# Optimization experiments

Hardware: AMD Instinct MI355X
Metric: run time of the kernel (lower is better)

The kernel has to match this reference:

```python
import jax, jax.numpy as jnp
import numpy as np

EMBED, HEADS, DEPTH = 1280, 16, 2
HD = EMBED // HEADS            # 80
MLP = 4 * EMBED                # 5120
HIDDEN = 3584
MERGE = 2
PATCH_IN = 3 * 2 * 14 * 14     # 1176
GRIDS = [(1, 32, 32), (1, 32, 32)]
SEQ = sum(t * h * w for t, h, w in GRIDS)  # 2048
THETA = 10000.0


def _pos_ids_np():
    m = MERGE
    out = []
    for t, h, w in GRIDS:
        hp = np.broadcast_to(np.arange(h)[:, None], (h, w))
        hp = hp.reshape(h // m, m, w // m, m).transpose(0, 2, 1, 3).reshape(-1)
        wp = np.broadcast_to(np.arange(w)[None, :], (h, w))
        wp = wp.reshape(h // m, m, w // m, m).transpose(0, 2, 1, 3).reshape(-1)
        out.append(np.tile(np.stack([hp, wp], -1), (t, 1)))
    return np.concatenate(out, 0).astype(np.int32)


def _cu_seqlens_np():
    lens = []
    for t, h, w in GRIDS:
        lens += [h * w] * t
    return np.concatenate([[0], np.cumsum(lens)]).astype(np.int32)


def setup_inputs() -> dict:
    key = jax.random.key(0)
    ks = iter(jax.random.split(key, 16))
    s = 0.02
    p = {}
    p["hidden_states"] = jax.random.normal(next(ks), (SEQ, PATCH_IN), jnp.float32)
    p["pos_ids"] = jnp.asarray(_pos_ids_np())
    p["cu_seqlens"] = jnp.asarray(_cu_seqlens_np())
    p["patch_w"] = jax.random.normal(next(ks), (PATCH_IN, EMBED)) * s
    p["ln1_w"] = jnp.ones((DEPTH, EMBED)); p["ln1_b"] = jnp.zeros((DEPTH, EMBED))
    p["ln2_w"] = jnp.ones((DEPTH, EMBED)); p["ln2_b"] = jnp.zeros((DEPTH, EMBED))
    p["qkv_w"] = jax.random.normal(next(ks), (DEPTH, EMBED, 3 * EMBED)) * s
    p["qkv_b"] = jnp.zeros((DEPTH, 3 * EMBED))
    p["proj_w"] = jax.random.normal(next(ks), (DEPTH, EMBED, EMBED)) * s
    p["proj_b"] = jnp.zeros((DEPTH, EMBED))
    p["fc1_w"] = jax.random.normal(next(ks), (DEPTH, EMBED, MLP)) * s
    p["fc1_b"] = jnp.zeros((DEPTH, MLP))
    p["fc2_w"] = jax.random.normal(next(ks), (DEPTH, MLP, EMBED)) * s
    p["fc2_b"] = jnp.zeros((DEPTH, EMBED))
    p["mrg_ln_w"] = jnp.ones((EMBED,)); p["mrg_ln_b"] = jnp.zeros((EMBED,))
    p["mrg_w1"] = jax.random.normal(next(ks), (EMBED * MERGE * MERGE, HIDDEN)) * s
    p["mrg_b1"] = jnp.zeros((HIDDEN,))
    p["mrg_w2"] = jax.random.normal(next(ks), (HIDDEN, HIDDEN)) * s
    p["mrg_b2"] = jnp.zeros((HIDDEN,))
    return p


def _ln(x, w, b, eps=1e-6):
    mu = jnp.mean(x, -1, keepdims=True)
    var = jnp.mean((x - mu) ** 2, -1, keepdims=True)
    return (x - mu) * jax.lax.rsqrt(var + eps) * w + b


def _rotate_half(x):
    x1, x2 = jnp.split(x, 2, axis=-1)
    return jnp.concatenate([-x2, x1], axis=-1)


def reference(hidden_states, pos_ids, cu_seqlens, patch_w, ln1_w, ln1_b, ln2_w,
              ln2_b, qkv_w, qkv_b, proj_w, proj_b, fc1_w, fc1_b, fc2_w, fc2_b,
              mrg_ln_w, mrg_ln_b, mrg_w1, mrg_b1, mrg_w2, mrg_b2):
    # patch embed (Conv3d with full-patch kernel == linear on flattened patch)
    x = hidden_states @ patch_w                              # [S, E]

    # vision rotary embedding over (h, w) position ids
    inv_freq = 1.0 / THETA ** (jnp.arange(0, HD // 2, 2, dtype=jnp.float32) / (HD // 2))  # [HD//4]
    freqs = pos_ids.astype(jnp.float32)[:, :, None] * inv_freq  # [S, 2, HD//4]
    freqs = freqs.reshape(SEQ, -1)                           # [S, HD//2]
    emb = jnp.concatenate([freqs, freqs], -1)                # [S, HD]
    cos = jnp.cos(emb)[:, None, :]
    sin = jnp.sin(emb)[:, None, :]

    # block-diagonal (per-image) mask from cu_seqlens
    seg = jnp.searchsorted(cu_seqlens[1:], jnp.arange(SEQ), side='right')
    mask = seg[:, None] == seg[None, :]                      # [S, S]

    scale = 1.0 / np.sqrt(HD)
    neg = jnp.finfo(jnp.float32).min
    for i in range(DEPTH):
        h = _ln(x, ln1_w[i], ln1_b[i])
        qkv = (h @ qkv_w[i] + qkv_b[i]).reshape(SEQ, 3, HEADS, HD)
        q, k, v = qkv[:, 0], qkv[:, 1], qkv[:, 2]
        q = q * cos + _rotate_half(q) * sin
        k = k * cos + _rotate_half(k) * sin
        scores = jnp.einsum('qhd,khd->hqk', q, k) * scale    # [H, S, S]
        scores = jnp.where(mask[None], scores, neg)
        attn = jax.nn.softmax(scores.astype(jnp.float32), -1).astype(q.dtype)
        o = jnp.einsum('hqk,khd->qhd', attn, v).reshape(SEQ, EMBED)
        x = x + o @ proj_w[i] + proj_b[i]
        h = _ln(x, ln2_w[i], ln2_b[i])
        x = x + jax.nn.silu(h @ fc1_w[i] + fc1_b[i]) @ fc2_w[i] + fc2_b[i]

    # patch merger: LN then merge 2x2 windows then 2-layer MLP
    y = _ln(x, mrg_ln_w, mrg_ln_b).reshape(-1, EMBED * MERGE * MERGE)
    y = jax.nn.gelu(y @ mrg_w1 + mrg_b1, approximate=False) @ mrg_w2 + mrg_b2
    return y                                                  # [S/4, HIDDEN]
```

## Files before the change

### kernel.cpp

```cpp
#include <hip/hip_runtime.h>
#include <math.h>

#define SEQ    2048
#define EMBED  1280
#define HEADS  16
#define HD     80
#define MLP    5120
#define HIDDEN 3584
#define QKVN   3840
#define SEGLEN 1024
#define NSEG   2
#define PATCH_IN 1176
#define PATCH_KP 1216
#define MROWS  512

typedef __attribute__((ext_vector_type(8))) short bf16x8;
typedef __attribute__((ext_vector_type(4))) float f32x4;
typedef unsigned short ushort_t;

__device__ __forceinline__ ushort_t f2bf(float f) {
    unsigned u = __builtin_bit_cast(unsigned, f);
    unsigned r = u + 0x7FFFu + ((u >> 16) & 1u);
    return (ushort_t)(r >> 16);
}

__device__ __forceinline__ void gld_lds16(const void* g, void* l) {
    __builtin_amdgcn_global_load_lds(
        (const __attribute__((address_space(1))) void*)g,
        (__attribute__((address_space(3))) void*)l, 16, 0, 0);
}

template<int EPI, int ACC, int OBF>
__global__ __launch_bounds__(256) void gemm_bf16(
    const ushort_t* __restrict__ A, const ushort_t* __restrict__ Bt,
    const float* __restrict__ bias, void* __restrict__ Cout,
    int M, int N, int K)
{
    __shared__ __align__(16) short Abuf[2][128 * 64];
    __shared__ __align__(16) short Bbuf[2][128 * 64];

    const int tid  = threadIdx.x;
    const int lane = tid & 63, wid = tid >> 6;
    const int wr = wid >> 1, wc = wid & 1;

    const int nwg  = gridDim.x * gridDim.y;
    const int flat = blockIdx.y * gridDim.x + blockIdx.x;
    int bx, by;
    if (nwg & 7) { bx = blockIdx.x; by = blockIdx.y; }
    else {
        const int swz = (flat & 7) * (nwg >> 3) + (flat >> 3);
        bx = swz % gridDim.x; by = swz / gridDim.x;
    }
    const int row0 = by * 128, col0 = bx * 128;

    const int r0 = tid >> 3, s0 = tid & 7;
    const int lrow = lane & 15;
    const int lg = lane >> 4;
    const int rx = lrow & 7;

    f32x4 acc[4][4] = {};

    auto stage = [&](int buf, int t) {
        const int k0 = t << 6;
        #pragma unroll
        for (int i = 0; i < 4; ++i) {
            const int r = r0 + i * 32;
            const int ksl = (s0 ^ (r & 7)) * 8;
            gld_lds16(A  + (size_t)(row0 + r) * K + k0 + ksl,
                      &Abuf[buf][(tid + i * 256) * 8]);
            gld_lds16(Bt + (size_t)(col0 + r) * K + k0 + ksl,
                      &Bbuf[buf][(tid + i * 256) * 8]);
        }
    };

    const int nt = K >> 6;
    stage(0, 0);
    stage(1, 1);

    int cur = 0;
    for (int t = 0; t < nt; ++t) {
        if (t < nt - 1) { asm volatile("s_waitcnt vmcnt(8)" ::: "memory"); }
        else            { asm volatile("s_waitcnt vmcnt(0)" ::: "memory"); }
        __builtin_amdgcn_s_barrier();

        bf16x8 a[2][4], b[2][4];
        #pragma unroll
        for (int ko = 0; ko < 2; ++ko) {
            const int ts = ((ko * 4 + lg) ^ rx) * 8;
            #pragma unroll
            for (int m = 0; m < 4; ++m)
                a[ko][m] = *(const bf16x8*)&Abuf[cur][(wr * 64 + m * 16 + lrow) * 64 + ts];
            #pragma unroll
            for (int n = 0; n < 4; ++n)
                b[ko][n] = *(const bf16x8*)&Bbuf[cur][(wc * 64 + n * 16 + lrow) * 64 + ts];
        }
        asm volatile("s_waitcnt lgkmcnt(0)" ::: "memory");
        __builtin_amdgcn_s_barrier();
        __builtin_amdgcn_sched_barrier(0);

        if (t + 2 < nt) stage(cur, t + 2);

        #pragma unroll
        for (int ko = 0; ko < 2; ++ko)
            #pragma unroll
            for (int m = 0; m < 4; ++m)
                #pragma unroll
                for (int n = 0; n < 4; ++n)
                    acc[m][n] = __builtin_amdgcn_mfma_f32_16x16x32_bf16(
                        a[ko][m], b[ko][n], acc[m][n], 0, 0, 0);
        cur ^= 1;
    }

    const int rbase = lg * 4;
    #pragma unroll
    for (int n = 0; n < 4; ++n) {
        const int c = col0 + wc * 64 + n * 16 + lrow;
        const float bv = bias ? bias[c] : 0.f;
        #pragma unroll
        for (int m = 0; m < 4; ++m) {
            const int rb = row0 + wr * 64 + m * 16 + rbase;
            #pragma unroll
            for (int g = 0; g < 4; ++g) {
                float v = acc[m][n][g] + bv;
                if (EPI == 1) v = v / (1.f + expf(-v));
                if (EPI == 2) v = 0.5f * v * (1.f + erff(v * 0.70710678f));
                const size_t idx = (size_t)(rb + g) * N + c;
                if (OBF) {
                    ((ushort_t*)Cout)[idx] = f2bf(v);
                } else {
                    float* Cf = (float*)Cout;
                    if (ACC) v += Cf[idx];
                    Cf[idx] = v;
                }
            }
        }
    }
}

__global__ __launch_bounds__(256) void transpose_cast(
    const float* __restrict__ in, ushort_t* __restrict__ out, int K, int N, int Kp)
{
    __shared__ float t[32][33];
    const int n0 = blockIdx.x * 32, k0 = blockIdx.y * 32;
    const int tx = threadIdx.x, ty = threadIdx.y;
    #pragma unroll
    for (int j = 0; j < 4; ++j) {
        int k = k0 + ty + j * 8;
        t[ty + j * 8][tx] = (k < K) ? in[(size_t)k * N + n0 + tx] : 0.f;
    }
    __syncthreads();
    #pragma unroll
    for (int j = 0; j < 4; ++j) {
        int n = n0 + ty + j * 8;
        out[(size_t)n * Kp + k0 + tx] = f2bf(t[tx][ty + j * 8]);
    }
}

__global__ __launch_bounds__(256) void cast_hs(
    const float* __restrict__ in, ushort_t* __restrict__ out)
{
    int idx = blockIdx.x * 256 + threadIdx.x;
    if (idx >= SEQ * PATCH_KP) return;
    int s = idx / PATCH_KP, k = idx % PATCH_KP;
    out[idx] = (k < PATCH_IN) ? f2bf(in[(size_t)s * PATCH_IN + k]) : 0;
}

__global__ __launch_bounds__(256) void ln_f32(
    const float* __restrict__ x, const float* __restrict__ w,
    const float* __restrict__ b, ushort_t* __restrict__ y, int D)
{
    const int row = blockIdx.x;
    const float* xr = x + (size_t)row * D;
    float s = 0.f, ss = 0.f;
    for (int d = threadIdx.x; d < D; d += 256) {
        float v = xr[d];
        s += v; ss = fmaf(v, v, ss);
    }
    __shared__ float red[2][4];
    const int lane = threadIdx.x & 63, wid = threadIdx.x >> 6;
    #pragma unroll
    for (int off = 32; off; off >>= 1) {
        s  += __shfl_xor(s,  off);
        ss += __shfl_xor(ss, off);
    }
    if (lane == 0) { red[0][wid] = s; red[1][wid] = ss; }
    __syncthreads();
    s  = red[0][0] + red[0][1] + red[0][2] + red[0][3];
    ss = red[1][0] + red[1][1] + red[1][2] + red[1][3];
    const float mu  = s / D;
    const float var = ss / D - mu * mu;
    const float inv = rsqrtf(var + 1e-6f);
    ushort_t* yr = y + (size_t)row * D;
    for (int d = threadIdx.x; d < D; d += 256)
        yr[d] = f2bf((xr[d] - mu) * inv * w[d] + b[d]);
}

__global__ __launch_bounds__(256) void rope_cast_qk(
    const float* __restrict__ qkv, const int* __restrict__ pos,
    ushort_t* __restrict__ qb, ushort_t* __restrict__ kb)
{
    int idx = blockIdx.x * 256 + threadIdx.x;
    const int j = idx % 48;
    const int h = (idx / 48) % HEADS;
    const int s = idx / (48 * HEADS);
    if (s >= SEQ) return;
    const size_t ob = ((size_t)h * SEQ + s) * 96;
    if (j >= 40) {
        qb[ob + 40 + j] = 0; qb[ob + 48 + j] = 0;
        kb[ob + 40 + j] = 0; kb[ob + 48 + j] = 0;
        return;
    }
    const float p = (float)pos[s * 2 + (j / 20)];
    const float f = p * powf(10000.f, -(float)(j % 20) / 20.f);
    float c, sn;
    sincosf(f, &c, &sn);
    const float* q = qkv + (size_t)s * QKVN + h * HD;
    const float* k = q + EMBED;
    const float scale = 0.11180339887498949f;
    float q1 = q[j], q2 = q[j + 40];
    qb[ob + j]      = f2bf((q1 * c - q2 * sn) * scale);
    qb[ob + j + 40] = f2bf((q2 * c + q1 * sn) * scale);
    float k1 = k[j], k2 = k[j + 40];
    kb[ob + j]      = f2bf(k1 * c - k2 * sn);
    kb[ob + j + 40] = f2bf(k2 * c + k1 * sn);
}

__global__ __launch_bounds__(256) void v_transpose(
    const float* __restrict__ qkv, ushort_t* __restrict__ vtb)
{
    int idx = blockIdx.x * 256 + threadIdx.x;
    int s = idx & (SEQ - 1);
    int d = (idx >> 11) % 80;
    int h = idx / (SEQ * 80);
    if (h >= HEADS) return;
    vtb[((size_t)h * 80 + d) * SEQ + s] =
        f2bf(qkv[(size_t)s * QKVN + 2 * EMBED + h * HD + d]);
}

#define AKC  64
#define KSTR 104
#define VSTR 72
#define PSTR 72

__global__ __launch_bounds__(256) void attn_mfma(
    const ushort_t* __restrict__ qb, const ushort_t* __restrict__ kb,
    const ushort_t* __restrict__ vtb, ushort_t* __restrict__ out)
{
    const int hh = blockIdx.x;
    const int seg = blockIdx.y;
    const int tid = threadIdx.x, lane = tid & 63, wid = tid >> 6;
    const int lr = lane & 15, lg = lane >> 4;

    __shared__ __align__(16) short Ks[AKC * KSTR];
    __shared__ __align__(16) short Vs[80 * VSTR];
    __shared__ __align__(16) short Ps[4][16 * PSTR];

    const int sq = seg * SEGLEN;
    const int qrow0 = sq + blockIdx.z * 64 + wid * 16;

    bf16x8 qf[3];
    #pragma unroll
    for (int f = 0; f < 3; ++f)
        qf[f] = *(const bf16x8*)&qb[((size_t)hh * SEQ + qrow0 + lr) * 96 + f * 32 + lg * 8];

    f32x4 o[5] = {};
    float m[4], l[4];
    #pragma unroll
    for (int g = 0; g < 4; ++g) { m[g] = -1e30f; l[g] = 0.f; }

    for (int c0 = 0; c0 < SEGLEN; c0 += AKC) {
        __syncthreads();
        #pragma unroll
        for (int i = 0; i < 3; ++i) {
            int id = tid + i * 256;
            int r = id / 12, s = id % 12;
            *(bf16x8*)&Ks[r * KSTR + s * 8] =
                *(const bf16x8*)&kb[((size_t)hh * SEQ + sq + c0 + r) * 96 + s * 8];
        }
        #pragma unroll
        for (int i = 0; i < 3; ++i) {
            int id = tid + i * 256;
            if (id < 640) {
                int d = id / 8, s = id % 8;
                *(bf16x8*)&Vs[d * VSTR + s * 8] =
                    *(const bf16x8*)&vtb[((size_t)hh * 80 + d) * SEQ + sq + c0 + s * 8];
            }
        }
        __syncthreads();

        f32x4 sc[4] = {};
        #pragma unroll
        for (int kt = 0; kt < 4; ++kt)
            #pragma unroll
            for (int f = 0; f < 3; ++f) {
                bf16x8 kf = *(const bf16x8*)&Ks[(kt * 16 + lr) * KSTR + f * 32 + lg * 8];
                sc[kt] = __builtin_amdgcn_mfma_f32_16x16x32_bf16(qf[f], kf, sc[kt], 0, 0, 0);
            }

        float corr[4], ps[4];
        #pragma unroll
        for (int g = 0; g < 4; ++g) {
            float v = fmaxf(fmaxf(sc[0][g], sc[1][g]), fmaxf(sc[2][g], sc[3][g]));
            v = fmaxf(v, __shfl_xor(v, 1));
            v = fmaxf(v, __shfl_xor(v, 2));
            v = fmaxf(v, __shfl_xor(v, 4));
            v = fmaxf(v, __shfl_xor(v, 8));
            const float mn = fmaxf(m[g], v);
            corr[g] = __expf(m[g] - mn);
            m[g] = mn;
            ps[g] = 0.f;
        }
        #pragma unroll
        for (int kt = 0; kt < 4; ++kt)
            #pragma unroll
            for (int g = 0; g < 4; ++g) {
                float p = __expf(sc[kt][g] - m[g]);
                ps[g] += p;
                Ps[wid][(lg * 4 + g) * PSTR + kt * 16 + lr] = f2bf(p);
            }
        #pragma unroll
        for (int g = 0; g < 4; ++g) {
            float rs = ps[g];
            rs += __shfl_xor(rs, 1);
            rs += __shfl_xor(rs, 2);
            rs += __shfl_xor(rs, 4);
            rs += __shfl_xor(rs, 8);
            l[g] = l[g] * corr[g] + rs;
        }
        #pragma unroll
        for (int n = 0; n < 5; ++n)
            #pragma unroll
            for (int g = 0; g < 4; ++g) o[n][g] *= corr[g];

        #pragma unroll
        for (int jf = 0; jf < 2; ++jf) {
            bf16x8 pa = *(const bf16x8*)&Ps[wid][lr * PSTR + jf * 32 + lg * 8];
            #pragma unroll
            for (int n = 0; n < 5; ++n) {
                bf16x8 vf = *(const bf16x8*)&Vs[(n * 16 + lr) * VSTR + jf * 32 + lg * 8];
                o[n] = __builtin_amdgcn_mfma_f32_16x16x32_bf16(pa, vf, o[n], 0, 0, 0);
            }
        }
    }

    #pragma unroll
    for (int g = 0; g < 4; ++g) {
        const float inv = 1.f / l[g];
        const int r = qrow0 + lg * 4 + g;
        #pragma unroll
        for (int n = 0; n < 5; ++n)
            out[(size_t)r * EMBED + hh * HD + n * 16 + lr] = f2bf(o[n][g] * inv);
    }
}


extern "C" void kernel_launch(void* const* d_in, const int* in_sizes, int n_in,
                              void* d_out, int out_size, void* d_ws, size_t ws_size,
                              hipStream_t stream)
{
    const float* hs      = (const float*)d_in[0];
    const int*   pos     = (const int*)  d_in[1];
    const float* patch_w = (const float*)d_in[3];
    const float* ln1_w   = (const float*)d_in[4];
    const float* ln1_b   = (const float*)d_in[5];
    const float* ln2_w   = (const float*)d_in[6];
    const float* ln2_b   = (const float*)d_in[7];
    const float* qkv_w   = (const float*)d_in[8];
    const float* qkv_b   = (const float*)d_in[9];
    const float* proj_w  = (const float*)d_in[10];
    const float* proj_b  = (const float*)d_in[11];
    const float* fc1_w   = (const float*)d_in[12];
    const float* fc1_b   = (const float*)d_in[13];
    const float* fc2_w   = (const float*)d_in[14];
    const float* fc2_b   = (const float*)d_in[15];
    const float* mln_w   = (const float*)d_in[16];
    const float* mln_b   = (const float*)d_in[17];
    const float* w1      = (const float*)d_in[18];
    const float* b1      = (const float*)d_in[19];
    const float* w2      = (const float*)d_in[20];
    const float* b2      = (const float*)d_in[21];
    float* out = (float*)d_out;

    char* p = (char*)d_ws;
    float*    x      = (float*)p;            p += (size_t)SEQ * EMBED * 4;
    float*    qkvbuf = (float*)p;            p += (size_t)SEQ * QKVN * 4;
    ushort_t* hbf    = (ushort_t*)p;         p += (size_t)SEQ * EMBED * 2;
    ushort_t* hsbf   = (ushort_t*)p;         p += (size_t)SEQ * PATCH_KP * 2;
    ushort_t* wbuf   = (ushort_t*)p;
    ushort_t* fc1out = (ushort_t*)qkvbuf;
    ushort_t* qbv = wbuf;
    ushort_t* kbv = qbv + (size_t)HEADS * SEQ * 96;
    ushort_t* vtb = kbv + (size_t)HEADS * SEQ * 96;

    const dim3 tblk(32, 8);
    auto tgrid = [](int N, int Kp) { return dim3(N / 32, Kp / 32); };
    auto ggrid = [](int M, int N) { return dim3(N / 128, M / 128); };

    cast_hs<<<(SEQ * PATCH_KP + 255) / 256, 256, 0, stream>>>(hs, hsbf);
    transpose_cast<<<tgrid(EMBED, PATCH_KP), tblk, 0, stream>>>(
        patch_w, wbuf, PATCH_IN, EMBED, PATCH_KP);
    gemm_bf16<0, 0, 0><<<ggrid(SEQ, EMBED), 256, 0, stream>>>(
        hsbf, wbuf, nullptr, x, SEQ, EMBED, PATCH_KP);

    for (int i = 0; i < 2; ++i) {
        ln_f32<<<SEQ, 256, 0, stream>>>(x, ln1_w + i * EMBED, ln1_b + i * EMBED, hbf, EMBED);
        transpose_cast<<<tgrid(QKVN, EMBED), tblk, 0, stream>>>(
            qkv_w + (size_t)i * EMBED * QKVN, wbuf, EMBED, QKVN, EMBED);
        gemm_bf16<0, 0, 0><<<ggrid(SEQ, QKVN), 256, 0, stream>>>(
            hbf, wbuf, qkv_b + i * QKVN, qkvbuf, SEQ, QKVN, EMBED);
        rope_cast_qk<<<SEQ * HEADS * 48 / 256, 256, 0, stream>>>(qkvbuf, pos, qbv, kbv);
        v_transpose<<<HEADS * 80 * SEQ / 256, 256, 0, stream>>>(qkvbuf, vtb);
        attn_mfma<<<dim3(HEADS, NSEG, SEGLEN / 64), 256, 0, stream>>>(qbv, kbv, vtb, hbf);
        transpose_cast<<<tgrid(EMBED, EMBED), tblk, 0, stream>>>(
            proj_w + (size_t)i * EMBED * EMBED, wbuf, EMBED, EMBED, EMBED);
        gemm_bf16<0, 1, 0><<<ggrid(SEQ, EMBED), 256, 0, stream>>>(
            hbf, wbuf, proj_b + i * EMBED, x, SEQ, EMBED, EMBED);
        ln_f32<<<SEQ, 256, 0, stream>>>(x, ln2_w + i * EMBED, ln2_b + i * EMBED, hbf, EMBED);
        transpose_cast<<<tgrid(MLP, EMBED), tblk, 0, stream>>>(
            fc1_w + (size_t)i * EMBED * MLP, wbuf, EMBED, MLP, EMBED);
        gemm_bf16<1, 0, 1><<<ggrid(SEQ, MLP), 256, 0, stream>>>(
            hbf, wbuf, fc1_b + i * MLP, fc1out, SEQ, MLP, EMBED);
        transpose_cast<<<tgrid(EMBED, MLP), tblk, 0, stream>>>(
            fc2_w + (size_t)i * MLP * EMBED, wbuf, MLP, EMBED, MLP);
        gemm_bf16<0, 1, 0><<<ggrid(SEQ, EMBED), 256, 0, stream>>>(
            fc1out, wbuf, fc2_b + i * EMBED, x, SEQ, EMBED, MLP);
    }

    ln_f32<<<SEQ, 256, 0, stream>>>(x, mln_w, mln_b, hbf, EMBED);
    transpose_cast<<<tgrid(HIDDEN, 4 * EMBED), tblk, 0, stream>>>(
        w1, wbuf, 4 * EMBED, HIDDEN, 4 * EMBED);
    gemm_bf16<2, 0, 1><<<ggrid(MROWS, HIDDEN), 256, 0, stream>>>(
        hbf, wbuf, b1, fc1out, MROWS, HIDDEN, 4 * EMBED);
    transpose_cast<<<tgrid(HIDDEN, HIDDEN), tblk, 0, stream>>>(
        w2, wbuf, HIDDEN, HIDDEN, HIDDEN);
    gemm_bf16<0, 0, 0><<<ggrid(MROWS, HIDDEN), 256, 0, stream>>>(
        fc1out, wbuf, b2, out, MROWS, HIDDEN, HIDDEN);
}
```

Baseline: 838.9 us.

## Add split-K with atomic accumulation to narrow GEMMs

Adds a SPLIT template parameter to the bf16 GEMM so the K dimension is divided across blockIdx.z. Partial sums are combined with float atomic adds, and the bias is added only by the z=0 slice. It is applied to the patch-embed, proj, fc2 and merger second GEMMs, whose N=1280/3584 grids give few workgroups. Output buffers that are not residual-accumulated are zeroed with memsets first, and PATCH_KP is padded to 1280 so it splits evenly. The aim is to fill more CUs, at the cost of atomic traffic, extra memsets and a nondeterministic summation order.

```diff
diff --git a/kernel.cpp b/kernel.cpp
--- a/kernel.cpp
+++ b/kernel.cpp
@@ -11,7 +11,7 @@
 #define SEGLEN 1024
 #define NSEG   2
 #define PATCH_IN 1176
-#define PATCH_KP 1216
+#define PATCH_KP 1280
 #define MROWS  512
 
 typedef __attribute__((ext_vector_type(8))) short bf16x8;
@@ -30,7 +30,7 @@
         (__attribute__((address_space(3))) void*)l, 16, 0, 0);
 }
 
-template<int EPI, int ACC, int OBF>
+template<int EPI, int ACC, int OBF, int SPLIT>
 __global__ __launch_bounds__(256) void gemm_bf16(
     const ushort_t* __restrict__ A, const ushort_t* __restrict__ Bt,
     const float* __restrict__ bias, void* __restrict__ Cout,
@@ -52,6 +52,8 @@
         bx = swz % gridDim.x; by = swz / gridDim.x;
     }
     const int row0 = by * 128, col0 = bx * 128;
+    const int kb = (SPLIT > 1) ? blockIdx.z * (K / SPLIT) : 0;
+    const int klen = (SPLIT > 1) ? (K / SPLIT) : K;
 
     const int r0 = tid >> 3, s0 = tid & 7;
     const int lrow = lane & 15;
@@ -61,7 +63,7 @@
     f32x4 acc[4][4] = {};
 
     auto stage = [&](int buf, int t) {
-        const int k0 = t << 6;
+        const int k0 = kb + (t << 6);
         #pragma unroll
         for (int i = 0; i < 4; ++i) {
             const int r = r0 + i * 32;
@@ -73,7 +75,7 @@
         }
     };
 
-    const int nt = K >> 6;
+    const int nt = klen >> 6;
     stage(0, 0);
     stage(1, 1);
 
@@ -121,16 +123,21 @@
             const int rb = row0 + wr * 64 + m * 16 + rbase;
             #pragma unroll
             for (int g = 0; g < 4; ++g) {
-                float v = acc[m][n][g] + bv;
-                if (EPI == 1) v = v / (1.f + expf(-v));
-                if (EPI == 2) v = 0.5f * v * (1.f + erff(v * 0.70710678f));
                 const size_t idx = (size_t)(rb + g) * N + c;
-                if (OBF) {
-                    ((ushort_t*)Cout)[idx] = f2bf(v);
+                if (SPLIT > 1) {
+                    float v = acc[m][n][g] + (blockIdx.z == 0 ? bv : 0.f);
+                    unsafeAtomicAdd(&((float*)Cout)[idx], v);
                 } else {
-                    float* Cf = (float*)Cout;
-                    if (ACC) v += Cf[idx];
-                    Cf[idx] = v;
+                    float v = acc[m][n][g] + bv;
+                    if (EPI == 1) v = v / (1.f + expf(-v));
+                    if (EPI == 2) v = 0.5f * v * (1.f + erff(v * 0.70710678f));
+                    if (OBF) {
+                        ((ushort_t*)Cout)[idx] = f2bf(v);
+                    } else {
+                        float* Cf = (float*)Cout;
+                        if (ACC) v += Cf[idx];
+                        Cf[idx] = v;
+                    }
                 }
             }
         }
@@ -394,45 +401,47 @@
 
     const dim3 tblk(32, 8);
     auto tgrid = [](int N, int Kp) { return dim3(N / 32, Kp / 32); };
-    auto ggrid = [](int M, int N) { return dim3(N / 128, M / 128); };
+    auto ggrid = [](int M, int N, int S = 1) { return dim3(N / 128, M / 128, S); };
 
     cast_hs<<<(SEQ * PATCH_KP + 255) / 256, 256, 0, stream>>>(hs, hsbf);
     transpose_cast<<<tgrid(EMBED, PATCH_KP), tblk, 0, stream>>>(
         patch_w, wbuf, PATCH_IN, EMBED, PATCH_KP);
-    gemm_bf16<0, 0, 0><<<ggrid(SEQ, EMBED), 256, 0, stream>>>(
+    hipMemsetAsync(x, 0, (size_t)SEQ * EMBED * 4, stream);
+    gemm_bf16<0, 0, 0, 2><<<ggrid(SEQ, EMBED, 2), 256, 0, stream>>>(
         hsbf, wbuf, nullptr, x, SEQ, EMBED, PATCH_KP);
 
     for (int i = 0; i < 2; ++i) {
         ln_f32<<<SEQ, 256, 0, stream>>>(x, ln1_w + i * EMBED, ln1_b + i * EMBED, hbf, EMBED);
         transpose_cast<<<tgrid(QKVN, EMBED), tblk, 0, stream>>>(
             qkv_w + (size_t)i * EMBED * QKVN, wbuf, EMBED, QKVN, EMBED);
-        gemm_bf16<0, 0, 0><<<ggrid(SEQ, QKVN), 256, 0, stream>>>(
+        gemm_bf16<0, 0, 0, 1><<<ggrid(SEQ, QKVN), 256, 0, stream>>>(
             hbf, wbuf, qkv_b + i * QKVN, qkvbuf, SEQ, QKVN, EMBED);
         rope_cast_qk<<<SEQ * HEADS * 48 / 256, 256, 0, stream>>>(qkvbuf, pos, qbv, kbv);
         v_transpose<<<HEADS * 80 * SEQ / 256, 256, 0, stream>>>(qkvbuf, vtb);
         attn_mfma<<<dim3(HEADS, NSEG, SEGLEN / 64), 256, 0, stream>>>(qbv, kbv, vtb, hbf);
         transpose_cast<<<tgrid(EMBED, EMBED), tblk, 0, stream>>>(
             proj_w + (size_t)i * EMBED * EMBED, wbuf, EMBED, EMBED, EMBED);
-        gemm_bf16<0, 1, 0><<<ggrid(SEQ, EMBED), 256, 0, stream>>>(
+        gemm_bf16<0, 1, 0, 2><<<ggrid(SEQ, EMBED, 2), 256, 0, stream>>>(
             hbf, wbuf, proj_b + i * EMBED, x, SEQ, EMBED, EMBED);
         ln_f32<<<SEQ, 256, 0, stream>>>(x, ln2_w + i * EMBED, ln2_b + i * EMBED, hbf, EMBED);
         transpose_cast<<<tgrid(MLP, EMBED), tblk, 0, stream>>>(
             fc1_w + (size_t)i * EMBED * MLP, wbuf, EMBED, MLP, EMBED);
-        gemm_bf16<1, 0, 1><<<ggrid(SEQ, MLP), 256, 0, stream>>>(
+        gemm_bf16<1, 0, 1, 1><<<ggrid(SEQ, MLP), 256, 0, stream>>>(
             hbf, wbuf, fc1_b + i * MLP, fc1out, SEQ, MLP, EMBED);
         transpose_cast<<<tgrid(EMBED, MLP), tblk, 0, stream>>>(
             fc2_w + (size_t)i * MLP * EMBED, wbuf, MLP, EMBED, MLP);
-        gemm_bf16<0, 1, 0><<<ggrid(SEQ, EMBED), 256, 0, stream>>>(
+        gemm_bf16<0, 1, 0, 4><<<ggrid(SEQ, EMBED, 4), 256, 0, stream>>>(
             fc1out, wbuf, fc2_b + i * EMBED, x, SEQ, EMBED, MLP);
     }
 
     ln_f32<<<SEQ, 256, 0, stream>>>(x, mln_w, mln_b, hbf, EMBED);
     transpose_cast<<<tgrid(HIDDEN, 4 * EMBED), tblk, 0, stream>>>(
         w1, wbuf, 4 * EMBED, HIDDEN, 4 * EMBED);
-    gemm_bf16<2, 0, 1><<<ggrid(MROWS, HIDDEN), 256, 0, stream>>>(
+    gemm_bf16<2, 0, 1, 1><<<ggrid(MROWS, HIDDEN), 256, 0, stream>>>(
         hbf, wbuf, b1, fc1out, MROWS, HIDDEN, 4 * EMBED);
     transpose_cast<<<tgrid(HIDDEN, HIDDEN), tblk, 0, stream>>>(
         w2, wbuf, HIDDEN, HIDDEN, HIDDEN);
-    gemm_bf16<0, 0, 0><<<ggrid(MROWS, HIDDEN), 256, 0, stream>>>(
+    hipMemsetAsync(out, 0, (size_t)MROWS * HIDDEN * 4, stream);
+    gemm_bf16<0, 0, 0, 4><<<ggrid(MROWS, HIDDEN, 4), 256, 0, stream>>>(
         fc1out, wbuf, b2, out, MROWS, HIDDEN, HIDDEN);
 }
```

Result: faster. 815.0 us (-2.9%).
